# Kernel tuning notes

Hardware: AMD Instinct MI355X
Metric: run time of the kernel (lower is better)

The kernel has to match this reference:

```python
import jax, jax.numpy as jnp
import numpy as np

# Dims: V = in-simplices, E = out-simplices, K = input_ch, C = target_ch,
#       D = in_depth_ch, O = o_depth_ch
V = 8192
E = 8192
K = 64
C = 64
D = 8
O = 8


def setup_inputs() -> dict:
    key = jax.random.key(0)
    k1, k2, k3, k4 = jax.random.split(key, 4)
    x = jax.random.normal(k1, (V, K, D), dtype=jnp.float32)
    G = jax.random.normal(k2, (E, V), dtype=jnp.float32) * 0.02  # dense boundary operator
    # o_depth_ch stacked TensorLinear weights: W[o, d, k, c], bias b[o, c, d]
    W = jax.random.normal(k3, (O, D, K, C), dtype=jnp.float32) * (1.0 / np.sqrt(K))
    b = jax.random.normal(k4, (O, C, D), dtype=jnp.float32) * 0.02
    return {"x": x, "G": G, "W": W, "b": b}


def reference(x, G, W, b):
    # Per out-depth channel o: y_o[v,c,d] = sum_k x[v,k,d] * W[o,d,k,c] + b[o,c,d]
    # output[e,c,o] = sum_{v,d} G[e,v] * y_o[v,c,d]
    # Fuse: sum over d inside the first contraction; bias contributes
    # rowsum(G)[e] * sum_d b[o,c,d].
    z = jnp.einsum('vkd,odkc->ovc', x, W) + b.sum(axis=-1)[:, None, :]  # [O, V, C]
    out = jnp.einsum('ev,ovc->eco', G, z)                               # [E, C, O]
    return out
```

## Files before the change

kernel.cpp:

```cpp
#include <hip/hip_runtime.h>
#include <hip/hip_bf16.h>

#define V_DIM 8192
#define E_DIM 8192
#define KD    512
#define CO    512

typedef __attribute__((ext_vector_type(8))) short short8;
typedef __attribute__((ext_vector_type(8))) unsigned short ushort8;
typedef __attribute__((ext_vector_type(4))) float f32x4;

__device__ __forceinline__ unsigned short f2b(float f) {
  __hip_bfloat16 h = __float2bfloat16(f);
  return __builtin_bit_cast(unsigned short, h);
}

__device__ __forceinline__ void gload_lds16(const void* g, void* l) {
  __builtin_amdgcn_global_load_lds(
      (const __attribute__((address_space(1))) void*)g,
      (__attribute__((address_space(3))) void*)l, 16, 0, 0);
}

__global__ void convert_x(const float* __restrict__ x, unsigned short* __restrict__ xb) {
  const size_t i = ((size_t)blockIdx.x * 256 + threadIdx.x) * 8;
  float4 f0 = *(const float4*)(x + i);
  float4 f1 = *(const float4*)(x + i + 4);
  ushort8 u;
  u[0]=f2b(f0.x); u[1]=f2b(f0.y); u[2]=f2b(f0.z); u[3]=f2b(f0.w);
  u[4]=f2b(f1.x); u[5]=f2b(f1.y); u[6]=f2b(f1.z); u[7]=f2b(f1.w);
  *(ushort8*)(xb + i) = u;
}

__global__ void repack_w(const float* __restrict__ W, const float* __restrict__ b,
                         float* __restrict__ Wt, float* __restrict__ bsum) {
  const int idx = blockIdx.x * 256 + threadIdx.x;
  const int j = idx >> 9, kd = idx & 511;
  const int c = j >> 3, o = j & 7, k = kd >> 3, d = kd & 7;
  Wt[idx] = W[(((o * 8 + d) * 64 + k) << 6) + c];
  if (idx < 512) {
    const int cc = idx >> 3, oo = idx & 7;
    float s = 0.f;
#pragma unroll
    for (int dd = 0; dd < 8; ++dd) s += b[((oo * 64 + cc) << 3) + dd];
    bsum[idx] = s;
  }
}

template<bool OUT_BF16, bool HASBIAS>
__global__ __launch_bounds__(512)
void gemm_bt(const float* __restrict__ A, const unsigned short* __restrict__ B,
             const float* __restrict__ bias, void* __restrict__ Cout,
             int ldA, int ldB, int ldC, int kdim) {
  __shared__ __align__(16) unsigned short As[2][128 * 64];
  __shared__ __align__(16) unsigned short Bs[2][128 * 64];

  const int tid  = threadIdx.x;
  const int lane = tid & 63;
  const int w    = tid >> 6;
  const int wm   = w >> 2;
  const int wn   = w & 3;
  const int m0   = blockIdx.y * 128;
  const int n0   = blockIdx.x * 128;

  const int sr  = tid >> 3;
  const int sc  = tid & 7;
  const int brl = lane >> 3;
  const int bch = lane & 7;

  f32x4 acc[4][2];
#pragma unroll
  for (int i = 0; i < 4; ++i)
#pragma unroll
    for (int j = 0; j < 2; ++j) acc[i][j] = (f32x4)0.0f;

  const int nT = kdim >> 6;

  auto stage = [&](int t, int buf) {
    const int kt = t << 6;
#pragma unroll
    for (int half = 0; half < 2; ++half) {
      const int row = sr + half * 64;
      const float* ag = A + (size_t)(m0 + row) * ldA + kt + sc * 8;
      float4 f0 = *(const float4*)ag;
      float4 f1 = *(const float4*)(ag + 4);
      ushort8 u;
      u[0]=f2b(f0.x); u[1]=f2b(f0.y); u[2]=f2b(f0.z); u[3]=f2b(f0.w);
      u[4]=f2b(f1.x); u[5]=f2b(f1.y); u[6]=f2b(f1.z); u[7]=f2b(f1.w);
      *(ushort8*)(&As[buf][row * 64 + ((sc ^ (row & 7)) * 8)]) = u;
    }
#pragma unroll
    for (int jr = 0; jr < 2; ++jr) {
      const int rbase = jr * 64 + w * 8;
      const int grow  = rbase + brl;
      const unsigned short* src =
          B + (size_t)(n0 + grow) * ldB + kt + ((bch ^ brl) * 8);
      gload_lds16(src, &Bs[buf][rbase * 64]);
    }
  };

  auto frag = [&](const unsigned short* S, int row, int chunk) -> short8 {
    return *(const short8*)(S + row * 64 + ((chunk ^ (row & 7)) * 8));
  };

  stage(0, 0);
  __syncthreads();
  int buf = 0;
  for (int t = 0; t < nT; ++t) {
    if (t + 1 < nT) stage(t + 1, buf ^ 1);
    const unsigned short* Ab = As[buf];
    const unsigned short* Bb = Bs[buf];
#pragma unroll
    for (int kk = 0; kk < 2; ++kk) {
      const int ck = kk * 4 + (lane >> 4);
      short8 a[4], b[2];
#pragma unroll
      for (int mi = 0; mi < 4; ++mi)
        a[mi] = frag(Ab, wm * 64 + mi * 16 + (lane & 15), ck);
#pragma unroll
      for (int ni = 0; ni < 2; ++ni)
        b[ni] = frag(Bb, wn * 32 + ni * 16 + (lane & 15), ck);
#pragma unroll
      for (int mi = 0; mi < 4; ++mi)
#pragma unroll
        for (int ni = 0; ni < 2; ++ni)
          acc[mi][ni] = __builtin_amdgcn_mfma_f32_16x16x32_bf16(
              a[mi], b[ni], acc[mi][ni], 0, 0, 0);
    }
    __syncthreads();
    buf ^= 1;
  }

  const int rg = lane >> 4;
  const int cl = lane & 15;
#pragma unroll
  for (int mi = 0; mi < 4; ++mi) {
#pragma unroll
    for (int r = 0; r < 4; ++r) {
      const int row = m0 + wm * 64 + mi * 16 + rg * 4 + r;
      float bv = 0.0f;
      if (HASBIAS) bv = bias[row];
#pragma unroll
      for (int ni = 0; ni < 2; ++ni) {
        const int col = n0 + wn * 32 + ni * 16 + cl;
        const float v = acc[mi][ni][r] + bv;
        if (OUT_BF16)
          ((unsigned short*)Cout)[(size_t)row * ldC + col] = f2b(v);
        else
          ((float*)Cout)[(size_t)row * ldC + col] = v;
      }
    }
  }
}

extern "C" void kernel_launch(void* const* d_in, const int* in_sizes, int n_in,
                              void* d_out, int out_size, void* d_ws, size_t ws_size,
                              hipStream_t stream) {
  const float* x = (const float*)d_in[0];
  const float* G = (const float*)d_in[1];
  const float* W = (const float*)d_in[2];
  const float* b = (const float*)d_in[3];

  char* ws = (char*)d_ws;
  unsigned short* xb = (unsigned short*)ws;
  float* Wt          = (float*)(ws + (8u << 20));
  float* bs          = (float*)(ws + (9u << 20));
  unsigned short* Zt = (unsigned short*)(ws + (9u << 20) + (1u << 16));

  hipLaunchKernelGGL(convert_x, dim3(2048), dim3(256), 0, stream, x, xb);
  hipLaunchKernelGGL(repack_w, dim3(1024), dim3(256), 0, stream, W, b, Wt, bs);

  hipLaunchKernelGGL((gemm_bt<true, true>), dim3(64, 4), dim3(512), 0, stream,
                     Wt, xb, bs, (void*)Zt, KD, KD, V_DIM, KD);

  hipLaunchKernelGGL((gemm_bt<false, false>), dim3(4, 64), dim3(512), 0, stream,
                     G, Zt, (const float*)nullptr, (void*)d_out,
                     V_DIM, V_DIM, CO, V_DIM);
}
```

Measured before the change: 552.7 us.

## Triple-buffer GEMM with register prefetch, explicit waitcnt pipeline and block swizzle

Replaces the double-buffered GEMM loop with a three-slot LDS pipeline. Global loads are issued two tiles ahead into registers, converted to bf16 one tile ahead, and guarded by explicit vmcnt/lgkmcnt waits and raw barriers. It also adds a block-index swizzle for the large G×Z GEMM to improve L2 reuse of the G rows and Z columns, and sets launch bounds to two blocks per CU. The aim is to hide global-load latency behind MFMA work, at the cost of more registers and LDS (96KB), which may prevent two blocks per CU from fitting.

```diff
diff --git a/kernel.cpp b/kernel.cpp
--- a/kernel.cpp
+++ b/kernel.cpp
@@ -46,89 +46,140 @@
   }
 }
 
-template<bool OUT_BF16, bool HASBIAS>
-__global__ __launch_bounds__(512)
+template<int NT, bool OUT_BF16, bool HASBIAS, bool SWIZ>
+__global__ __launch_bounds__(512, 2)
 void gemm_bt(const float* __restrict__ A, const unsigned short* __restrict__ B,
              const float* __restrict__ bias, void* __restrict__ Cout,
-             int ldA, int ldB, int ldC, int kdim) {
-  __shared__ __align__(16) unsigned short As[2][128 * 64];
-  __shared__ __align__(16) unsigned short Bs[2][128 * 64];
+             int ldA, int ldB, int ldC) {
+  static_assert((NT - 2) % 6 == 0, "pipeline needs (NT-2) divisible by 6");
+  __shared__ __align__(16) unsigned short As[3][128 * 64];
+  __shared__ __align__(16) unsigned short Bs[3][128 * 64];
 
   const int tid  = threadIdx.x;
   const int lane = tid & 63;
   const int w    = tid >> 6;
   const int wm   = w >> 2;
   const int wn   = w & 3;
-  const int m0   = blockIdx.y * 128;
-  const int n0   = blockIdx.x * 128;
+
+  int bm, bn;
+  if (SWIZ) {
+    int bid = blockIdx.x + (blockIdx.y << 2);
+    bid = ((bid & 7) << 5) | (bid >> 3);
+    bm = bid >> 2; bn = bid & 3;
+  } else {
+    bm = blockIdx.y; bn = blockIdx.x;
+  }
+  const int m0 = bm * 128, n0 = bn * 128;
 
   const int sr  = tid >> 3;
   const int sc  = tid & 7;
   const int brl = lane >> 3;
   const int bch = lane & 7;
 
+  const float* agB0 = A + (size_t)(m0 + sr) * ldA + sc * 8;
+  const float* agB1 = agB0 + (size_t)64 * ldA;
+  const int aw0 = sr * 64 + ((sc ^ (sr & 7)) * 8);
+  const int aw1 = aw0 + 64 * 64;
+
+  const unsigned short* bsrc0 =
+      B + (size_t)(n0 + w * 8 + brl) * ldB + ((bch ^ brl) * 8);
+  const unsigned short* bsrc1 = bsrc0 + (size_t)64 * ldB;
+  const int bd0 = (w * 8) * 64;
+  const int bd1 = (64 + w * 8) * 64;
+
   f32x4 acc[4][2];
 #pragma unroll
   for (int i = 0; i < 4; ++i)
 #pragma unroll
     for (int j = 0; j < 2; ++j) acc[i][j] = (f32x4)0.0f;
 
-  const int nT = kdim >> 6;
-
-  auto stage = [&](int t, int buf) {
-    const int kt = t << 6;
-#pragma unroll
-    for (int half = 0; half < 2; ++half) {
-      const int row = sr + half * 64;
-      const float* ag = A + (size_t)(m0 + row) * ldA + kt + sc * 8;
-      float4 f0 = *(const float4*)ag;
-      float4 f1 = *(const float4*)(ag + 4);
-      ushort8 u;
-      u[0]=f2b(f0.x); u[1]=f2b(f0.y); u[2]=f2b(f0.z); u[3]=f2b(f0.w);
-      u[4]=f2b(f1.x); u[5]=f2b(f1.y); u[6]=f2b(f1.z); u[7]=f2b(f1.w);
-      *(ushort8*)(&As[buf][row * 64 + ((sc ^ (row & 7)) * 8)]) = u;
+  f32x4 pf[2][4];
+
+#define STAGE_LOAD(T, C, SLOT) do {                                       \
+    const int kt_ = (T) << 6;                                             \
+    pf[(C)][0] = *(const f32x4*)(agB0 + kt_);                             \
+    pf[(C)][1] = *(const f32x4*)(agB0 + kt_ + 4);                         \
+    pf[(C)][2] = *(const f32x4*)(agB1 + kt_);                             \
+    pf[(C)][3] = *(const f32x4*)(agB1 + kt_ + 4);                         \
+    gload_lds16(bsrc0 + kt_, &Bs[(SLOT)][bd0]);                           \
+    gload_lds16(bsrc1 + kt_, &Bs[(SLOT)][bd1]);                           \
+  } while (0)
+
+#define STAGE_WRITE(C, SLOT) do {                                         \
+    ushort8 u0_, u1_;                                                     \
+    u0_[0]=f2b(pf[(C)][0][0]); u0_[1]=f2b(pf[(C)][0][1]);                 \
+    u0_[2]=f2b(pf[(C)][0][2]); u0_[3]=f2b(pf[(C)][0][3]);                 \
+    u0_[4]=f2b(pf[(C)][1][0]); u0_[5]=f2b(pf[(C)][1][1]);                 \
+    u0_[6]=f2b(pf[(C)][1][2]); u0_[7]=f2b(pf[(C)][1][3]);                 \
+    u1_[0]=f2b(pf[(C)][2][0]); u1_[1]=f2b(pf[(C)][2][1]);                 \
+    u1_[2]=f2b(pf[(C)][2][2]); u1_[3]=f2b(pf[(C)][2][3]);                 \
+    u1_[4]=f2b(pf[(C)][3][0]); u1_[5]=f2b(pf[(C)][3][1]);                 \
+    u1_[6]=f2b(pf[(C)][3][2]); u1_[7]=f2b(pf[(C)][3][3]);                 \
+    *(ushort8*)(&As[(SLOT)][aw0]) = u0_;                                  \
+    *(ushort8*)(&As[(SLOT)][aw1]) = u1_;                                  \
+  } while (0)
+
+#define COMPUTE(SLOT) do {                                                \
+    const unsigned short* Ab_ = As[(SLOT)];                               \
+    const unsigned short* Bb_ = Bs[(SLOT)];                               \
+    _Pragma("unroll")                                                     \
+    for (int kk = 0; kk < 2; ++kk) {                                      \
+      const int ck_ = kk * 4 + (lane >> 4);                               \
+      short8 af_[4], bf_[2];                                              \
+      _Pragma("unroll")                                                   \
+      for (int mi = 0; mi < 4; ++mi) {                                    \
+        const int r_ = wm * 64 + mi * 16 + (lane & 15);                   \
+        af_[mi] = *(const short8*)(Ab_ + r_ * 64 + ((ck_ ^ (r_ & 7)) * 8)); \
+      }                                                                   \
+      _Pragma("unroll")                                                   \
+      for (int ni = 0; ni < 2; ++ni) {                                    \
+        const int r_ = wn * 32 + ni * 16 + (lane & 15);                   \
+        bf_[ni] = *(const short8*)(Bb_ + r_ * 64 + ((ck_ ^ (r_ & 7)) * 8)); \
+      }                                                                   \
+      _Pragma("unroll")                                                   \
+      for (int mi = 0; mi < 4; ++mi)                                      \
+        _Pragma("unroll")                                                 \
+        for (int ni = 0; ni < 2; ++ni)                                    \
+          acc[mi][ni] = __builtin_amdgcn_mfma_f32_16x16x32_bf16(          \
+              af_[mi], bf_[ni], acc[mi][ni], 0, 0, 0);                    \
+    }                                                                     \
+  } while (0)
+
+  STAGE_LOAD(0, 0, 0);
+  STAGE_LOAD(1, 1, 1);
+  STAGE_WRITE(0, 0);
+
+#pragma unroll 1
+  for (int tb = 0; tb < NT - 2; tb += 6) {
+#pragma unroll
+    for (int jj = 0; jj < 6; ++jj) {
+      STAGE_LOAD(tb + jj + 2, jj & 1, (jj + 2) % 3);
+      asm volatile("s_waitcnt vmcnt(6)" ::: "memory");
+      STAGE_WRITE((jj + 1) & 1, (jj + 1) % 3);
+      asm volatile("s_waitcnt lgkmcnt(0)" ::: "memory");
+      __builtin_amdgcn_sched_barrier(0);
+      __builtin_amdgcn_s_barrier();
+      __builtin_amdgcn_sched_barrier(0);
+      COMPUTE(jj % 3);
+      __builtin_amdgcn_sched_barrier(0);
+      __builtin_amdgcn_s_barrier();
     }
-#pragma unroll
-    for (int jr = 0; jr < 2; ++jr) {
-      const int rbase = jr * 64 + w * 8;
-      const int grow  = rbase + brl;
-      const unsigned short* src =
-          B + (size_t)(n0 + grow) * ldB + kt + ((bch ^ brl) * 8);
-      gload_lds16(src, &Bs[buf][rbase * 64]);
-    }
-  };
-
-  auto frag = [&](const unsigned short* S, int row, int chunk) -> short8 {
-    return *(const short8*)(S + row * 64 + ((chunk ^ (row & 7)) * 8));
-  };
-
-  stage(0, 0);
-  __syncthreads();
-  int buf = 0;
-  for (int t = 0; t < nT; ++t) {
-    if (t + 1 < nT) stage(t + 1, buf ^ 1);
-    const unsigned short* Ab = As[buf];
-    const unsigned short* Bb = Bs[buf];
-#pragma unroll
-    for (int kk = 0; kk < 2; ++kk) {
-      const int ck = kk * 4 + (lane >> 4);
-      short8 a[4], b[2];
-#pragma unroll
-      for (int mi = 0; mi < 4; ++mi)
-        a[mi] = frag(Ab, wm * 64 + mi * 16 + (lane & 15), ck);
-#pragma unroll
-      for (int ni = 0; ni < 2; ++ni)
-        b[ni] = frag(Bb, wn * 32 + ni * 16 + (lane & 15), ck);
-#pragma unroll
-      for (int mi = 0; mi < 4; ++mi)
-#pragma unroll
-        for (int ni = 0; ni < 2; ++ni)
-          acc[mi][ni] = __builtin_amdgcn_mfma_f32_16x16x32_bf16(
-              a[mi], b[ni], acc[mi][ni], 0, 0, 0);
-    }
-    __syncthreads();
-    buf ^= 1;
-  }
+  }
+
+  asm volatile("s_waitcnt vmcnt(0)" ::: "memory");
+  STAGE_WRITE((NT - 1) & 1, (NT - 1) % 3);
+  asm volatile("s_waitcnt lgkmcnt(0)" ::: "memory");
+  __builtin_amdgcn_sched_barrier(0);
+  __builtin_amdgcn_s_barrier();
+  __builtin_amdgcn_sched_barrier(0);
+  COMPUTE((NT - 2) % 3);
+  __builtin_amdgcn_sched_barrier(0);
+  __builtin_amdgcn_s_barrier();
+  COMPUTE((NT - 1) % 3);
+
+#undef STAGE_LOAD
+#undef STAGE_WRITE
+#undef COMPUTE
 
   const int rg = lane >> 4;
   const int cl = lane & 15;
@@ -169,10 +220,10 @@
   hipLaunchKernelGGL(convert_x, dim3(2048), dim3(256), 0, stream, x, xb);
   hipLaunchKernelGGL(repack_w, dim3(1024), dim3(256), 0, stream, W, b, Wt, bs);
 
-  hipLaunchKernelGGL((gemm_bt<true, true>), dim3(64, 4), dim3(512), 0, stream,
-                     Wt, xb, bs, (void*)Zt, KD, KD, V_DIM, KD);
-
-  hipLaunchKernelGGL((gemm_bt<false, false>), dim3(4, 64), dim3(512), 0, stream,
-                     G, Zt, (const float*)nullptr, (void*)d_out,
-                     V_DIM, V_DIM, CO, V_DIM);
-}
+  hipLaunchKernelGGL((gemm_bt<8, true, true, false>), dim3(64, 4), dim3(512), 0,
+                     stream, Wt, xb, bs, (void*)Zt, KD, KD, V_DIM);
+
+  hipLaunchKernelGGL((gemm_bt<128, false, false, true>), dim3(4, 64), dim3(512), 0,
+                     stream, G, Zt, (const float*)nullptr, (void*)d_out,
+                     V_DIM, V_DIM, CO);
+}
```

After: 502.9 us. 1.1x faster.
